# Optimization experiments

Hardware: AMD Instinct MI355X
Metric: run time of the kernel (lower is better)

Reference implementation:

```python
import jax, jax.numpy as jnp
from jax import lax
import numpy as np

D_MODEL = 512
D_INNER = 1024      # expand=2
D_STATE = 256       # min(512, 256)
D_CONV = 4
DT_RANK = 32        # ceil(512/16)
N_FUSED = 64
EPS = 1e-5


def setup_inputs() -> dict:
    key = jax.random.key(0)
    ks = jax.random.split(key, 14)
    B, Lx = 4, 2048
    s = lambda k, shape: (jax.random.normal(k, shape, jnp.float32) * 0.02)
    return {
        "x": jax.random.normal(ks[0], (B, Lx, D_MODEL), jnp.float32),
        "fused_tokens": jax.random.normal(ks[1], (1, N_FUSED, D_MODEL), jnp.float32),
        "g1": jnp.ones((D_MODEL,), jnp.float32),
        "b1": jnp.zeros((D_MODEL,), jnp.float32),
        "g2": jnp.ones((D_MODEL,), jnp.float32),
        "b2": jnp.zeros((D_MODEL,), jnp.float32),
        "W_head": s(ks[2], (D_MODEL, D_MODEL)),
        "b_head": jnp.zeros((D_MODEL,), jnp.float32),
        "W_in": s(ks[3], (2 * D_INNER, D_MODEL)),          # in_proj, bias=False
        "W_conv": s(ks[4], (D_INNER, D_CONV)),             # depthwise causal conv
        "b_conv": s(ks[5], (D_INNER,)),
        "W_xp": s(ks[6], (DT_RANK + 2 * D_STATE, D_INNER)),  # x_proj, bias=False
        "W_dt": s(ks[7], (D_INNER, DT_RANK)),
        "b_dt": s(ks[8], (D_INNER,)),
        "A_log": jnp.log(jnp.broadcast_to(
            jnp.arange(1, D_STATE + 1, dtype=jnp.float32), (D_INNER, D_STATE))),
        "Dp": jnp.ones((D_INNER,), jnp.float32),           # skip parameter D
        "W_out": s(ks[9], (D_MODEL, D_INNER)),             # out_proj, bias=False
    }


def _ln(t, g, b):
    m = t.mean(-1, keepdims=True)
    v = t.var(-1, keepdims=True)
    return (t - m) * lax.rsqrt(v + EPS) * g + b


def _causal_dwconv(x, w, b):
    # x: (B, L, D); w: (D, K) depthwise kernel
    K = w.shape[1]
    xp = jnp.pad(x, ((0, 0), (K - 1, 0), (0, 0)))
    y = lax.conv_general_dilated(
        xp.transpose(0, 2, 1), w[:, None, :], (1,), 'VALID',
        feature_group_count=w.shape[0],
        dimension_numbers=('NCH', 'OIH', 'NCH'))
    return y.transpose(0, 2, 1) + b


def _selective_scan(u, delta, A, Bm, Cm, Dp):
    # u, delta: (B, L, Din); Bm, Cm: (B, L, N); A: (Din, N)
    B_, L, Din = u.shape
    N = A.shape[1]

    def step(h, inp):
        u_t, d_t, B_t, C_t = inp            # (B,Din),(B,Din),(B,N),(B,N)
        dA = jnp.exp(d_t[..., None] * A)    # (B, Din, N)
        h = dA * h + (d_t * u_t)[..., None] * B_t[:, None, :]
        y = jnp.einsum('bdn,bn->bd', h, C_t)
        return h, y

    h0 = jnp.zeros((B_, Din, N), u.dtype)
    xs = (u.transpose(1, 0, 2), delta.transpose(1, 0, 2),
          Bm.transpose(1, 0, 2), Cm.transpose(1, 0, 2))
    _, ys = lax.scan(step, h0, xs)
    return ys.transpose(1, 0, 2) + u * Dp


def reference(x, fused_tokens, g1, b1, g2, b2, W_head, b_head, W_in,
              W_conv, b_conv, W_xp, W_dt, b_dt, A_log, Dp, W_out):
    B = x.shape[0]
    toks = jnp.broadcast_to(fused_tokens, (B,) + fused_tokens.shape[1:])
    h = jnp.concatenate([x, toks], axis=1)          # (B, L, d)

    # --- Mamba block with pre-LN residual ---
    a = _ln(h, g1, b1)
    xz = a @ W_in.T                                 # (B, L, 2*Din)
    u, z = jnp.split(xz, 2, axis=-1)
    u = jax.nn.silu(_causal_dwconv(u, W_conv, b_conv))
    dbl = u @ W_xp.T                                # (B, L, dt_rank + 2N)
    dt, Bm, Cm = jnp.split(dbl, [DT_RANK, DT_RANK + D_STATE], axis=-1)
    delta = jax.nn.softplus(dt @ W_dt.T + b_dt)     # (B, L, Din)
    A = -jnp.exp(A_log)
    y = _selective_scan(u, delta, A, Bm, Cm, Dp)
    y = y * jax.nn.silu(z)
    h = y @ W_out.T + h

    # --- head with pre-LN residual ---
    h = _ln(h, g2, b2) @ W_head.T + b_head + h

    return h[:, -N_FUSED:, :]
```

## Files before the change

kernel.cpp:

```cpp
#include <hip/hip_runtime.h>

#define LTOT 2112
#define NROWS 8448
#define DM 512
#define DIN 1024
#define NST 256

using short8 = short  __attribute__((ext_vector_type(8)));
using f32x4  = float  __attribute__((ext_vector_type(4)));

__device__ __forceinline__ float fast_silu(float x){ return x / (1.f + __expf(-x)); }

__device__ __forceinline__ unsigned short f2bf(float f){
  unsigned u = __float_as_uint(f);
  unsigned r = (u + 0x7FFFu + ((u >> 16) & 1u)) >> 16;
  return (unsigned short)r;
}

__global__ __launch_bounds__(256) void ln1_kernel(
    const float* __restrict__ x, const float* __restrict__ toks,
    const float* __restrict__ g1, const float* __restrict__ b1,
    float* __restrict__ a, unsigned short* __restrict__ abf)
{
  int r = blockIdx.x;
  int bb = r / LTOT, t = r - bb*LTOT;
  const float* row = (t < 2048) ? (x + ((size_t)bb*2048 + t)*DM)
                                : (toks + (size_t)(t - 2048)*DM);
  int tid = threadIdx.x;
  float v0 = row[tid], v1 = row[tid + 256];
  float s = v0 + v1, sq = v0*v0 + v1*v1;
  #pragma unroll
  for (int o = 32; o > 0; o >>= 1){ s += __shfl_down(s,o); sq += __shfl_down(sq,o); }
  __shared__ float sb[8];
  if ((tid & 63) == 0){ sb[tid>>6] = s; sb[4 + (tid>>6)] = sq; }
  __syncthreads();
  float S  = sb[0]+sb[1]+sb[2]+sb[3];
  float SQ = sb[4]+sb[5]+sb[6]+sb[7];
  float mean = S * (1.f/DM);
  float var  = SQ * (1.f/DM) - mean*mean;
  float rs = rsqrtf(var + 1e-5f);
  size_t o0 = (size_t)r*DM;
  float r0 = (v0 - mean)*rs*g1[tid]       + b1[tid];
  float r1 = (v1 - mean)*rs*g1[tid + 256] + b1[tid + 256];
  a[o0 + tid]       = r0;
  a[o0 + tid + 256] = r1;
  abf[o0 + tid]       = f2bf(r0);
  abf[o0 + tid + 256] = f2bf(r1);
}

__global__ __launch_bounds__(256) void f32_to_bf16_kernel(
    const float* __restrict__ in, unsigned short* __restrict__ out, int n4)
{
  int i = blockIdx.x*256 + threadIdx.x;
  if (i >= n4) return;
  float4 v = reinterpret_cast<const float4*>(in)[i];
  ushort4 o;
  o.x = f2bf(v.x); o.y = f2bf(v.y); o.z = f2bf(v.z); o.w = f2bf(v.w);
  reinterpret_cast<ushort4*>(out)[i] = o;
}

__global__ __launch_bounds__(256) void gemm_bf16(
    const unsigned short* __restrict__ A, const unsigned short* __restrict__ W,
    float* __restrict__ C, int M, int N, int K, int ldc)
{
  __shared__ unsigned short As[128][40];
  __shared__ unsigned short Bs[64][40];
  int tid  = threadIdx.x;
  int lane = tid & 63, wid = tid >> 6;
  int wm = wid >> 1, wn = wid & 1;
  int l15 = lane & 15, l4 = lane >> 4;
  int m0 = blockIdx.x * 128, n0 = blockIdx.y * 64;
  int sr = tid >> 2, sc = (tid & 3) * 8;

  f32x4 acc[4][2];
  #pragma unroll
  for (int i = 0; i < 4; ++i)
    #pragma unroll
    for (int j = 0; j < 2; ++j) acc[i][j] = (f32x4)0.f;

  for (int k0 = 0; k0 < K; k0 += 32) {
    #pragma unroll
    for (int rr = 0; rr < 2; ++rr) {
      int r = sr + rr*64;
      uint4 v = *reinterpret_cast<const uint4*>(A + (size_t)(m0 + r)*K + k0 + sc);
      *reinterpret_cast<uint4*>(&As[r][sc]) = v;
    }
    {
      int col = n0 + sr;
      uint4 v = make_uint4(0u,0u,0u,0u);
      if (col < N) v = *reinterpret_cast<const uint4*>(W + (size_t)col*K + k0 + sc);
      *reinterpret_cast<uint4*>(&Bs[sr][sc]) = v;
    }
    __syncthreads();
    short8 bfrag[2];
    #pragma unroll
    for (int fn = 0; fn < 2; ++fn)
      bfrag[fn] = *reinterpret_cast<const short8*>(&Bs[wn*32 + fn*16 + l15][l4*8]);
    #pragma unroll
    for (int fm = 0; fm < 4; ++fm) {
      short8 afrag = *reinterpret_cast<const short8*>(&As[wm*64 + fm*16 + l15][l4*8]);
      acc[fm][0] = __builtin_amdgcn_mfma_f32_16x16x32_bf16(afrag, bfrag[0], acc[fm][0], 0, 0, 0);
      acc[fm][1] = __builtin_amdgcn_mfma_f32_16x16x32_bf16(afrag, bfrag[1], acc[fm][1], 0, 0, 0);
    }
    __syncthreads();
  }
  #pragma unroll
  for (int fm = 0; fm < 4; ++fm)
    #pragma unroll
    for (int fn = 0; fn < 2; ++fn) {
      int col = n0 + wn*32 + fn*16 + l15;
      if (col < N)
        #pragma unroll
        for (int j = 0; j < 4; ++j) {
          int row = m0 + wm*64 + fm*16 + l4*4 + j;
          C[(size_t)row*ldc + col] = acc[fm][fn][j];
        }
    }
}

__global__ __launch_bounds__(256) void z_rows_kernel(
    const float* __restrict__ a, const float* __restrict__ Wz, float* __restrict__ zs)
{
  int rr = blockIdx.x;
  int bb = rr >> 6, tt = rr & 63;
  size_t r = (size_t)bb*LTOT + 2048 + tt;
  __shared__ float as[DM];
  int tid = threadIdx.x;
  as[tid]       = a[r*DM + tid];
  as[tid + 256] = a[r*DM + tid + 256];
  __syncthreads();
  #pragma unroll
  for (int cj = 0; cj < 4; ++cj) {
    int cidx = tid + cj*256;
    const float* wr = Wz + (size_t)cidx*DM;
    float acc = 0.f;
    for (int k = 0; k < DM; k += 4) {
      float4 w4 = *reinterpret_cast<const float4*>(wr + k);
      float4 a4 = *reinterpret_cast<const float4*>(&as[k]);
      acc = fmaf(a4.x,w4.x,acc); acc = fmaf(a4.y,w4.y,acc);
      acc = fmaf(a4.z,w4.z,acc); acc = fmaf(a4.w,w4.w,acc);
    }
    zs[(size_t)rr*DIN + cidx] = fast_silu(acc);
  }
}

__global__ __launch_bounds__(256) void conv_silu_kernel(
    const float* __restrict__ upre, const float* __restrict__ Wc,
    const float* __restrict__ bc, float* __restrict__ u, unsigned short* __restrict__ ubf)
{
  size_t idx = (size_t)blockIdx.x*256 + threadIdx.x;
  int d = (int)(idx & 1023);
  int r = (int)(idx >> 10);
  int t = r % LTOT;
  float4 w4 = *reinterpret_cast<const float4*>(Wc + (size_t)d*4);
  float acc = bc[d];
  const float* up = upre + idx;
  if (t >= 3) acc = fmaf(up[-3*DIN], w4.x, acc);
  if (t >= 2) acc = fmaf(up[-2*DIN], w4.y, acc);
  if (t >= 1) acc = fmaf(up[-1*DIN], w4.z, acc);
  acc = fmaf(up[0], w4.w, acc);
  float res = fast_silu(acc);
  u[idx] = res;
  ubf[idx] = f2bf(res);
}

__global__ __launch_bounds__(256) void c_rows_kernel(
    const float* __restrict__ u, const float* __restrict__ Wxp, float* __restrict__ Cm)
{
  int rr = blockIdx.x;
  int bb = rr >> 6, tt = rr & 63;
  size_t r = (size_t)bb*LTOT + 2048 + tt;
  __shared__ float us[DIN];
  int tid = threadIdx.x;
  #pragma unroll
  for (int j = 0; j < 4; ++j) us[tid + j*256] = u[r*DIN + tid + j*256];
  __syncthreads();
  const float* wr = Wxp + (size_t)(288 + tid)*DIN;
  float acc = 0.f;
  for (int k = 0; k < DIN; k += 4) {
    float4 w4 = *reinterpret_cast<const float4*>(wr + k);
    float4 a4 = *reinterpret_cast<const float4*>(&us[k]);
    acc = fmaf(a4.x,w4.x,acc); acc = fmaf(a4.y,w4.y,acc);
    acc = fmaf(a4.z,w4.z,acc); acc = fmaf(a4.w,w4.w,acc);
  }
  Cm[(size_t)rr*NST + tid] = acc;
}

__global__ __launch_bounds__(256) void delta_kernel(
    const float* __restrict__ dbl, const float* __restrict__ W_dt,
    const float* __restrict__ b_dt, const float* __restrict__ u,
    float* __restrict__ deltaT, float* __restrict__ duT)
{
  __shared__ float dts[32][33];
  __shared__ float wds[32][33];
  __shared__ float dT[32][33];
  __shared__ float uT[32][33];
  int r0 = blockIdx.x * 32;
  int d0 = blockIdx.y * 32;
  int bb = r0 / LTOT, t0 = r0 % LTOT;
  int tid = threadIdx.x;
  #pragma unroll
  for (int p = 0; p < 4; ++p) {
    int o = tid + p*256;
    int rl = o >> 5, j = o & 31;
    dts[rl][j] = dbl[(size_t)(r0 + rl)*288 + j];
    wds[rl][j] = W_dt[(size_t)(d0 + rl)*32 + j];
  }
  __syncthreads();
  #pragma unroll
  for (int p = 0; p < 4; ++p) {
    int o = tid + p*256;
    int dl = o & 31, rl = o >> 5;
    float acc = b_dt[d0 + dl];
    #pragma unroll
    for (int j = 0; j < 32; ++j) acc = fmaf(dts[rl][j], wds[dl][j], acc);
    float delta = (acc > 20.f) ? acc : __logf(1.f + __expf(acc));
    float uu = u[(size_t)(r0 + rl)*DIN + d0 + dl];
    dT[dl][rl] = delta;
    uT[dl][rl] = delta * uu;
  }
  __syncthreads();
  #pragma unroll
  for (int p = 0; p < 4; ++p) {
    int o = tid + p*256;
    int dl = o >> 5, ti = o & 31;
    size_t gi = ((size_t)bb*DIN + d0 + dl)*LTOT + t0 + ti;
    deltaT[gi] = dT[dl][ti];
    duT[gi]    = uT[dl][ti];
  }
}

__global__ __launch_bounds__(256) void scan_kernel(
    const float* __restrict__ deltaT, const float* __restrict__ duT,
    const float* __restrict__ dbl, const float* __restrict__ Cm,
    const float* __restrict__ A_log, float* __restrict__ y)
{
  int blk = blockIdx.x;
  int bb = blk >> 8;
  int d0 = (blk & 255) << 2;
  int n = threadIdx.x;
  float Ak[4], h[4] = {0.f,0.f,0.f,0.f};
  #pragma unroll
  for (int g = 0; g < 4; ++g) {
    float al = A_log[(size_t)(d0+g)*NST + n];
    Ak[g] = -__builtin_amdgcn_exp2f(al * 1.44269504089f) * 1.44269504089f;
  }
  const size_t basebd = ((size_t)bb*DIN + d0)*LTOT;
  const float* __restrict__ pd = deltaT + basebd;
  const float* __restrict__ pu = duT    + basebd;
  const float* __restrict__ Bp = dbl + (size_t)bb*LTOT*288 + 32 + n;

  for (int t0c = 0; t0c < 2048; t0c += 4) {
    float Bnv[4];
    #pragma unroll
    for (int i = 0; i < 4; ++i) Bnv[i] = Bp[(size_t)(t0c + i)*288];
    float dv[4][4], uv[4][4];
    #pragma unroll
    for (int g = 0; g < 4; ++g) {
      float4 dq = *reinterpret_cast<const float4*>(pd + (size_t)g*LTOT + t0c);
      float4 uq = *reinterpret_cast<const float4*>(pu + (size_t)g*LTOT + t0c);
      dv[g][0]=dq.x; dv[g][1]=dq.y; dv[g][2]=dq.z; dv[g][3]=dq.w;
      uv[g][0]=uq.x; uv[g][1]=uq.y; uv[g][2]=uq.z; uv[g][3]=uq.w;
    }
    #pragma unroll
    for (int i = 0; i < 4; ++i) {
      float Bn = Bnv[i];
      #pragma unroll
      for (int g = 0; g < 4; ++g) {
        float dA = __builtin_amdgcn_exp2f(dv[g][i] * Ak[g]);
        h[g] = fmaf(dA, h[g], uv[g][i] * Bn);
      }
    }
  }

  __shared__ float red[4][4];
  for (int t = 2048; t < 2112; ++t) {
    float Bn = Bp[(size_t)t*288];
    #pragma unroll
    for (int g = 0; g < 4; ++g) {
      float dA = __builtin_amdgcn_exp2f(pd[(size_t)g*LTOT + t] * Ak[g]);
      h[g] = fmaf(dA, h[g], pu[(size_t)g*LTOT + t] * Bn);
    }
    float Cn = Cm[((size_t)(bb*64 + (t - 2048)))*NST + n];
    #pragma unroll
    for (int g = 0; g < 4; ++g) {
      float v = h[g] * Cn;
      #pragma unroll
      for (int o = 32; o > 0; o >>= 1) v += __shfl_down(v, o);
      if ((threadIdx.x & 63) == 0) red[threadIdx.x >> 6][g] = v;
    }
    __syncthreads();
    if (threadIdx.x < 4) {
      float sv = red[0][threadIdx.x] + red[1][threadIdx.x]
               + red[2][threadIdx.x] + red[3][threadIdx.x];
      y[((size_t)(bb*64 + (t - 2048)))*DIN + d0 + threadIdx.x] = sv;
    }
    __syncthreads();
  }
}

__global__ __launch_bounds__(256) void y2_kernel(
    const float* __restrict__ y, const float* __restrict__ u, const float* __restrict__ zs,
    const float* __restrict__ Dp, float* __restrict__ y2)
{
  int idx = blockIdx.x*256 + threadIdx.x;
  int rr = idx >> 10, d = idx & 1023;
  int bb = rr >> 6, tt = rr & 63;
  size_t r = (size_t)bb*LTOT + 2048 + tt;
  float yv = y[idx] + u[r*DIN + d] * Dp[d];
  y2[idx] = yv * zs[idx];
}

__global__ __launch_bounds__(256) void outproj_kernel(
    const float* __restrict__ y2, const float* __restrict__ Wout,
    const float* __restrict__ toks, float* __restrict__ hfin)
{
  __shared__ float ys[4][DIN];
  int rb = blockIdx.x;
  int tid = threadIdx.x;
  #pragma unroll
  for (int rr = 0; rr < 4; ++rr)
    #pragma unroll
    for (int j = 0; j < 4; ++j)
      ys[rr][tid + j*256] = y2[(size_t)(rb*4 + rr)*DIN + tid + j*256];
  __syncthreads();
  #pragma unroll
  for (int cj = 0; cj < 2; ++cj) {
    int cidx = tid + cj*256;
    const float* wr = Wout + (size_t)cidx*DIN;
    float a0=0.f,a1=0.f,a2=0.f,a3=0.f;
    for (int k = 0; k < DIN; k += 4) {
      float4 w4 = *reinterpret_cast<const float4*>(wr + k);
      float4 r0 = *reinterpret_cast<const float4*>(&ys[0][k]);
      float4 r1 = *reinterpret_cast<const float4*>(&ys[1][k]);
      float4 r2 = *reinterpret_cast<const float4*>(&ys[2][k]);
      float4 r3 = *reinterpret_cast<const float4*>(&ys[3][k]);
      a0=fmaf(r0.x,w4.x,a0); a0=fmaf(r0.y,w4.y,a0); a0=fmaf(r0.z,w4.z,a0); a0=fmaf(r0.w,w4.w,a0);
      a1=fmaf(r1.x,w4.x,a1); a1=fmaf(r1.y,w4.y,a1); a1=fmaf(r1.z,w4.z,a1); a1=fmaf(r1.w,w4.w,a1);
      a2=fmaf(r2.x,w4.x,a2); a2=fmaf(r2.y,w4.y,a2); a2=fmaf(r2.z,w4.z,a2); a2=fmaf(r2.w,w4.w,a2);
      a3=fmaf(r3.x,w4.x,a3); a3=fmaf(r3.y,w4.y,a3); a3=fmaf(r3.z,w4.z,a3); a3=fmaf(r3.w,w4.w,a3);
    }
    float accs[4] = {a0,a1,a2,a3};
    #pragma unroll
    for (int rr = 0; rr < 4; ++rr) {
      int rg = rb*4 + rr;
      hfin[(size_t)rg*DM + cidx] = accs[rr] + toks[(size_t)(rg & 63)*DM + cidx];
    }
  }
}

__global__ __launch_bounds__(256) void head_kernel(
    const float* __restrict__ hfin, const float* __restrict__ g2, const float* __restrict__ b2,
    const float* __restrict__ Wh, const float* __restrict__ bh, float* __restrict__ out)
{
  int rr = blockIdx.x;
  int tid = threadIdx.x;
  float v0 = hfin[(size_t)rr*DM + tid];
  float v1 = hfin[(size_t)rr*DM + tid + 256];
  float s = v0 + v1, sq = v0*v0 + v1*v1;
  #pragma unroll
  for (int o = 32; o > 0; o >>= 1){ s += __shfl_down(s,o); sq += __shfl_down(sq,o); }
  __shared__ float sb[8];
  if ((tid & 63) == 0){ sb[tid>>6] = s; sb[4 + (tid>>6)] = sq; }
  __syncthreads();
  float S  = sb[0]+sb[1]+sb[2]+sb[3];
  float SQ = sb[4]+sb[5]+sb[6]+sb[7];
  float mean = S * (1.f/DM);
  float rs = rsqrtf(SQ * (1.f/DM) - mean*mean + 1e-5f);
  __shared__ float as[DM];
  as[tid]       = (v0 - mean)*rs*g2[tid]       + b2[tid];
  as[tid + 256] = (v1 - mean)*rs*g2[tid + 256] + b2[tid + 256];
  __syncthreads();
  #pragma unroll
  for (int cj = 0; cj < 2; ++cj) {
    int cidx = tid + cj*256;
    const float* wr = Wh + (size_t)cidx*DM;
    float acc = bh[cidx] + (cj ? v1 : v0);
    for (int k = 0; k < DM; k += 4) {
      float4 w4 = *reinterpret_cast<const float4*>(wr + k);
      float4 a4 = *reinterpret_cast<const float4*>(&as[k]);
      acc = fmaf(a4.x,w4.x,acc); acc = fmaf(a4.y,w4.y,acc);
      acc = fmaf(a4.z,w4.z,acc); acc = fmaf(a4.w,w4.w,acc);
    }
    out[(size_t)rr*DM + cidx] = acc;
  }
}

extern "C" void kernel_launch(void* const* d_in, const int* in_sizes, int n_in,
                              void* d_out, int out_size, void* d_ws, size_t ws_size,
                              hipStream_t stream) {
  const float* x      = (const float*)d_in[0];
  const float* toks   = (const float*)d_in[1];
  const float* g1     = (const float*)d_in[2];
  const float* b1     = (const float*)d_in[3];
  const float* g2     = (const float*)d_in[4];
  const float* b2     = (const float*)d_in[5];
  const float* W_head = (const float*)d_in[6];
  const float* b_head = (const float*)d_in[7];
  const float* W_in   = (const float*)d_in[8];
  const float* W_conv = (const float*)d_in[9];
  const float* b_conv = (const float*)d_in[10];
  const float* W_xp   = (const float*)d_in[11];
  const float* W_dt   = (const float*)d_in[12];
  const float* b_dt   = (const float*)d_in[13];
  const float* A_log  = (const float*)d_in[14];
  const float* Dp     = (const float*)d_in[15];
  const float* W_out  = (const float*)d_in[16];

  float* ws = (float*)d_ws;
  float* a_buf   = ws;
  float* u_pre   = a_buf   + (size_t)NROWS*DM;
  float* u_buf   = u_pre   + (size_t)NROWS*DIN;
  float* dbl_buf = u_buf   + (size_t)NROWS*DIN;
  float* duT     = dbl_buf + (size_t)NROWS*288;
  float* zs      = duT     + (size_t)NROWS*DIN;
  float* Cm      = zs      + (size_t)256*DIN;
  float* y_buf   = Cm      + (size_t)256*NST;
  float* y2_buf  = y_buf   + (size_t)256*DIN;
  float* hfin    = y2_buf  + (size_t)256*DIN;
  float* deltaT  = u_pre;

  unsigned short* a_bf16  = (unsigned short*)duT;
  unsigned short* u_bf16  = a_bf16 + (size_t)NROWS*DM;
  unsigned short* wi_bf16 = u_bf16 + (size_t)NROWS*DIN;
  unsigned short* wx_bf16 = wi_bf16 + (size_t)DIN*DM;

  f32_to_bf16_kernel<<<(DIN*DM/4 + 255)/256, 256, 0, stream>>>(W_in, wi_bf16, DIN*DM/4);
  f32_to_bf16_kernel<<<(288*DIN/4 + 255)/256, 256, 0, stream>>>(W_xp, wx_bf16, 288*DIN/4);

  ln1_kernel<<<NROWS, 256, 0, stream>>>(x, toks, g1, b1, a_buf, a_bf16);
  gemm_bf16<<<dim3(NROWS/128, DIN/64), 256, 0, stream>>>(a_bf16, wi_bf16, u_pre,
                                                         NROWS, DIN, DM, DIN);
  z_rows_kernel<<<256, 256, 0, stream>>>(a_buf, W_in + (size_t)DIN*DM, zs);
  conv_silu_kernel<<<(NROWS*DIN)/256, 256, 0, stream>>>(u_pre, W_conv, b_conv, u_buf, u_bf16);
  gemm_bf16<<<dim3(NROWS/128, (288 + 63)/64), 256, 0, stream>>>(u_bf16, wx_bf16, dbl_buf,
                                                                NROWS, 288, DIN, 288);
  c_rows_kernel<<<256, 256, 0, stream>>>(u_buf, W_xp, Cm);
  delta_kernel<<<dim3(NROWS/32, DIN/32), 256, 0, stream>>>(dbl_buf, W_dt, b_dt, u_buf,
                                                           deltaT, duT);
  scan_kernel<<<1024, 256, 0, stream>>>(deltaT, duT, dbl_buf, Cm, A_log, y_buf);
  y2_kernel<<<1024, 256, 0, stream>>>(y_buf, u_buf, zs, Dp, y2_buf);
  outproj_kernel<<<64, 256, 0, stream>>>(y2_buf, W_out, toks, hfin);
  head_kernel<<<256, 256, 0, stream>>>(hfin, g2, b2, W_head, b_head, (float*)d_out);
}
```

Measured before the change: 839.7 us.

## Use bf16 MFMA GEMMs for z/C tail rows and halve scan channels per block

Replaces the scalar fp32 z_rows and c_rows kernels with small bf16 MFMA GEMM launches over the last 64 tokens per batch. LN1 and conv emit compact bf16 copies of those rows, and the weight conversion now covers the full W_in and W_xp. SiLU on z moves into y2_kernel. The scan kernel processes 2 channels per block instead of 4, doubling the grid to 2048 blocks for more parallelism, at the cost of more redundant B loads and less work per thread. The z and C projections now run in bf16, which lowers their precision.

```diff
diff --git a/kernel.cpp b/kernel.cpp
--- a/kernel.cpp
+++ b/kernel.cpp
@@ -20,7 +20,8 @@
 __global__ __launch_bounds__(256) void ln1_kernel(
     const float* __restrict__ x, const float* __restrict__ toks,
     const float* __restrict__ g1, const float* __restrict__ b1,
-    float* __restrict__ a, unsigned short* __restrict__ abf)
+    float* __restrict__ a, unsigned short* __restrict__ abf,
+    unsigned short* __restrict__ a_last)
 {
   int r = blockIdx.x;
   int bb = r / LTOT, t = r - bb*LTOT;
@@ -44,8 +45,14 @@
   float r1 = (v1 - mean)*rs*g1[tid + 256] + b1[tid + 256];
   a[o0 + tid]       = r0;
   a[o0 + tid + 256] = r1;
-  abf[o0 + tid]       = f2bf(r0);
-  abf[o0 + tid + 256] = f2bf(r1);
+  unsigned short h0 = f2bf(r0), h1 = f2bf(r1);
+  abf[o0 + tid]       = h0;
+  abf[o0 + tid + 256] = h1;
+  if (t >= 2048) {
+    size_t lr = (size_t)(bb*64 + (t - 2048))*DM;
+    a_last[lr + tid]       = h0;
+    a_last[lr + tid + 256] = h1;
+  }
 }
 
 __global__ __launch_bounds__(256) void f32_to_bf16_kernel(
@@ -118,35 +125,10 @@
     }
 }
 
-__global__ __launch_bounds__(256) void z_rows_kernel(
-    const float* __restrict__ a, const float* __restrict__ Wz, float* __restrict__ zs)
-{
-  int rr = blockIdx.x;
-  int bb = rr >> 6, tt = rr & 63;
-  size_t r = (size_t)bb*LTOT + 2048 + tt;
-  __shared__ float as[DM];
-  int tid = threadIdx.x;
-  as[tid]       = a[r*DM + tid];
-  as[tid + 256] = a[r*DM + tid + 256];
-  __syncthreads();
-  #pragma unroll
-  for (int cj = 0; cj < 4; ++cj) {
-    int cidx = tid + cj*256;
-    const float* wr = Wz + (size_t)cidx*DM;
-    float acc = 0.f;
-    for (int k = 0; k < DM; k += 4) {
-      float4 w4 = *reinterpret_cast<const float4*>(wr + k);
-      float4 a4 = *reinterpret_cast<const float4*>(&as[k]);
-      acc = fmaf(a4.x,w4.x,acc); acc = fmaf(a4.y,w4.y,acc);
-      acc = fmaf(a4.z,w4.z,acc); acc = fmaf(a4.w,w4.w,acc);
-    }
-    zs[(size_t)rr*DIN + cidx] = fast_silu(acc);
-  }
-}
-
 __global__ __launch_bounds__(256) void conv_silu_kernel(
     const float* __restrict__ upre, const float* __restrict__ Wc,
-    const float* __restrict__ bc, float* __restrict__ u, unsigned short* __restrict__ ubf)
+    const float* __restrict__ bc, float* __restrict__ u,
+    unsigned short* __restrict__ ubf, unsigned short* __restrict__ u_last)
 {
   size_t idx = (size_t)blockIdx.x*256 + threadIdx.x;
   int d = (int)(idx & 1023);
@@ -161,29 +143,12 @@
   acc = fmaf(up[0], w4.w, acc);
   float res = fast_silu(acc);
   u[idx] = res;
-  ubf[idx] = f2bf(res);
-}
-
-__global__ __launch_bounds__(256) void c_rows_kernel(
-    const float* __restrict__ u, const float* __restrict__ Wxp, float* __restrict__ Cm)
-{
-  int rr = blockIdx.x;
-  int bb = rr >> 6, tt = rr & 63;
-  size_t r = (size_t)bb*LTOT + 2048 + tt;
-  __shared__ float us[DIN];
-  int tid = threadIdx.x;
-  #pragma unroll
-  for (int j = 0; j < 4; ++j) us[tid + j*256] = u[r*DIN + tid + j*256];
-  __syncthreads();
-  const float* wr = Wxp + (size_t)(288 + tid)*DIN;
-  float acc = 0.f;
-  for (int k = 0; k < DIN; k += 4) {
-    float4 w4 = *reinterpret_cast<const float4*>(wr + k);
-    float4 a4 = *reinterpret_cast<const float4*>(&us[k]);
-    acc = fmaf(a4.x,w4.x,acc); acc = fmaf(a4.y,w4.y,acc);
-    acc = fmaf(a4.z,w4.z,acc); acc = fmaf(a4.w,w4.w,acc);
-  }
-  Cm[(size_t)rr*NST + tid] = acc;
+  unsigned short hb = f2bf(res);
+  ubf[idx] = hb;
+  if (t >= 2048) {
+    int bb = r / LTOT;
+    u_last[(size_t)(bb*64 + (t - 2048))*DIN + d] = hb;
+  }
 }
 
 __global__ __launch_bounds__(256) void delta_kernel(
@@ -236,12 +201,12 @@
     const float* __restrict__ A_log, float* __restrict__ y)
 {
   int blk = blockIdx.x;
-  int bb = blk >> 8;
-  int d0 = (blk & 255) << 2;
+  int bb = blk >> 9;
+  int d0 = (blk & 511) << 1;
   int n = threadIdx.x;
-  float Ak[4], h[4] = {0.f,0.f,0.f,0.f};
-  #pragma unroll
-  for (int g = 0; g < 4; ++g) {
+  float Ak[2], h[2] = {0.f, 0.f};
+  #pragma unroll
+  for (int g = 0; g < 2; ++g) {
     float al = A_log[(size_t)(d0+g)*NST + n];
     Ak[g] = -__builtin_amdgcn_exp2f(al * 1.44269504089f) * 1.44269504089f;
   }
@@ -254,9 +219,9 @@
     float Bnv[4];
     #pragma unroll
     for (int i = 0; i < 4; ++i) Bnv[i] = Bp[(size_t)(t0c + i)*288];
-    float dv[4][4], uv[4][4];
-    #pragma unroll
-    for (int g = 0; g < 4; ++g) {
+    float dv[2][4], uv[2][4];
+    #pragma unroll
+    for (int g = 0; g < 2; ++g) {
       float4 dq = *reinterpret_cast<const float4*>(pd + (size_t)g*LTOT + t0c);
       float4 uq = *reinterpret_cast<const float4*>(pu + (size_t)g*LTOT + t0c);
       dv[g][0]=dq.x; dv[g][1]=dq.y; dv[g][2]=dq.z; dv[g][3]=dq.w;
@@ -266,31 +231,31 @@
     for (int i = 0; i < 4; ++i) {
       float Bn = Bnv[i];
       #pragma unroll
-      for (int g = 0; g < 4; ++g) {
+      for (int g = 0; g < 2; ++g) {
         float dA = __builtin_amdgcn_exp2f(dv[g][i] * Ak[g]);
         h[g] = fmaf(dA, h[g], uv[g][i] * Bn);
       }
     }
   }
 
-  __shared__ float red[4][4];
+  __shared__ float red[4][2];
   for (int t = 2048; t < 2112; ++t) {
     float Bn = Bp[(size_t)t*288];
     #pragma unroll
-    for (int g = 0; g < 4; ++g) {
+    for (int g = 0; g < 2; ++g) {
       float dA = __builtin_amdgcn_exp2f(pd[(size_t)g*LTOT + t] * Ak[g]);
       h[g] = fmaf(dA, h[g], pu[(size_t)g*LTOT + t] * Bn);
     }
     float Cn = Cm[((size_t)(bb*64 + (t - 2048)))*NST + n];
     #pragma unroll
-    for (int g = 0; g < 4; ++g) {
+    for (int g = 0; g < 2; ++g) {
       float v = h[g] * Cn;
       #pragma unroll
       for (int o = 32; o > 0; o >>= 1) v += __shfl_down(v, o);
       if ((threadIdx.x & 63) == 0) red[threadIdx.x >> 6][g] = v;
     }
     __syncthreads();
-    if (threadIdx.x < 4) {
+    if (threadIdx.x < 2) {
       float sv = red[0][threadIdx.x] + red[1][threadIdx.x]
                + red[2][threadIdx.x] + red[3][threadIdx.x];
       y[((size_t)(bb*64 + (t - 2048)))*DIN + d0 + threadIdx.x] = sv;
@@ -308,7 +273,7 @@
   int bb = rr >> 6, tt = rr & 63;
   size_t r = (size_t)bb*LTOT + 2048 + tt;
   float yv = y[idx] + u[r*DIN + d] * Dp[d];
-  y2[idx] = yv * zs[idx];
+  y2[idx] = yv * fast_silu(zs[idx]);
 }
 
 __global__ __launch_bounds__(256) void outproj_kernel(
@@ -418,27 +383,34 @@
   float* y_buf   = Cm      + (size_t)256*NST;
   float* y2_buf  = y_buf   + (size_t)256*DIN;
   float* hfin    = y2_buf  + (size_t)256*DIN;
+  float* tail    = hfin    + (size_t)256*DM;
   float* deltaT  = u_pre;
+
+  unsigned short* a_last_bf16 = (unsigned short*)tail;
+  unsigned short* u_last_bf16 = a_last_bf16 + (size_t)256*DM;
 
   unsigned short* a_bf16  = (unsigned short*)duT;
   unsigned short* u_bf16  = a_bf16 + (size_t)NROWS*DM;
   unsigned short* wi_bf16 = u_bf16 + (size_t)NROWS*DIN;
-  unsigned short* wx_bf16 = wi_bf16 + (size_t)DIN*DM;
-
-  f32_to_bf16_kernel<<<(DIN*DM/4 + 255)/256, 256, 0, stream>>>(W_in, wi_bf16, DIN*DM/4);
-  f32_to_bf16_kernel<<<(288*DIN/4 + 255)/256, 256, 0, stream>>>(W_xp, wx_bf16, 288*DIN/4);
-
-  ln1_kernel<<<NROWS, 256, 0, stream>>>(x, toks, g1, b1, a_buf, a_bf16);
+  unsigned short* wx_bf16 = wi_bf16 + (size_t)2*DIN*DM;
+
+  f32_to_bf16_kernel<<<(2*DIN*DM/4 + 255)/256, 256, 0, stream>>>(W_in, wi_bf16, 2*DIN*DM/4);
+  f32_to_bf16_kernel<<<(544*DIN/4 + 255)/256, 256, 0, stream>>>(W_xp, wx_bf16, 544*DIN/4);
+
+  ln1_kernel<<<NROWS, 256, 0, stream>>>(x, toks, g1, b1, a_buf, a_bf16, a_last_bf16);
   gemm_bf16<<<dim3(NROWS/128, DIN/64), 256, 0, stream>>>(a_bf16, wi_bf16, u_pre,
                                                          NROWS, DIN, DM, DIN);
-  z_rows_kernel<<<256, 256, 0, stream>>>(a_buf, W_in + (size_t)DIN*DM, zs);
-  conv_silu_kernel<<<(NROWS*DIN)/256, 256, 0, stream>>>(u_pre, W_conv, b_conv, u_buf, u_bf16);
+  gemm_bf16<<<dim3(2, DIN/64), 256, 0, stream>>>(a_last_bf16, wi_bf16 + (size_t)DIN*DM,
+                                                 zs, 256, DIN, DM, DIN);
+  conv_silu_kernel<<<(NROWS*DIN)/256, 256, 0, stream>>>(u_pre, W_conv, b_conv,
+                                                        u_buf, u_bf16, u_last_bf16);
   gemm_bf16<<<dim3(NROWS/128, (288 + 63)/64), 256, 0, stream>>>(u_bf16, wx_bf16, dbl_buf,
                                                                 NROWS, 288, DIN, 288);
-  c_rows_kernel<<<256, 256, 0, stream>>>(u_buf, W_xp, Cm);
+  gemm_bf16<<<dim3(2, NST/64), 256, 0, stream>>>(u_last_bf16, wx_bf16 + (size_t)288*DIN,
+                                                 Cm, 256, NST, DIN, NST);
   delta_kernel<<<dim3(NROWS/32, DIN/32), 256, 0, stream>>>(dbl_buf, W_dt, b_dt, u_buf,
                                                            deltaT, duT);
-  scan_kernel<<<1024, 256, 0, stream>>>(deltaT, duT, dbl_buf, Cm, A_log, y_buf);
+  scan_kernel<<<2048, 256, 0, stream>>>(deltaT, duT, dbl_buf, Cm, A_log, y_buf);
   y2_kernel<<<1024, 256, 0, stream>>>(y_buf, u_buf, zs, Dp, y2_buf);
   outproj_kernel<<<64, 256, 0, stream>>>(y2_buf, W_out, toks, hfin);
   head_kernel<<<256, 256, 0, stream>>>(hfin, g2, b2, W_head, b_head, (float*)d_out);
```

Result: faster. 709.1 us (-15.6%).
